# Kernel tuning notes

Measured on AMD Instinct MI355X. Metric: run time of the kernel, lower is better.

The kernel has to match this reference:

```python
import jax, jax.numpy as jnp
import numpy as np

B, S, W, D, H = 2, 2048, 32, 1024, 16

def setup_inputs() -> dict:
    key = jax.random.key(0)
    ks = jax.random.split(key, 8)
    scale = 0.02
    return {
        'q': jax.random.normal(ks[0], (B, S, D), jnp.float32),
        'k': jax.random.normal(ks[1], (B, S, W, D), jnp.float32),
        'v': jax.random.normal(ks[2], (B, S, W, D), jnp.float32),
        'Wq': jax.random.normal(ks[3], (D, D), jnp.float32) * scale,
        'bq': jnp.zeros((D,), jnp.float32),
        'Wk': jax.random.normal(ks[4], (D, D), jnp.float32) * scale,
        'bk': jnp.zeros((D,), jnp.float32),
        'Wv': jax.random.normal(ks[5], (D, D), jnp.float32) * scale,
        'bv': jnp.zeros((D,), jnp.float32),
        'Wo': jax.random.normal(ks[6], (D, D), jnp.float32) * scale,
        'bo': jnp.zeros((D,), jnp.float32),
        'num_heads': H,
    }

def reference(q, k, v, Wq, bq, Wk, bk, Wv, bv, Wo, bo, num_heads):
    b, s, d = q.shape
    w = k.shape[2]
    hd = d // num_heads
    # query: Linear -> view(B,S,H,1,hd) -> transpose(1,2) => (B,H,S,1,hd)
    qh = (q @ Wq.T + bq).reshape(b, s, num_heads, 1, hd).transpose(0, 2, 1, 3, 4)
    # key/value: Linear then RAW view (B,H,S,W,hd) -- faithful to torch .view (no head transpose)
    kh = (k @ Wk.T + bk).reshape(b, num_heads, s, w, hd)
    vh = (v @ Wv.T + bv).reshape(b, num_heads, s, w, hd)
    # scores: (B,H,S,1,W), scaled by sqrt(head_dim) (query.shape[-1] inside attention)
    scores = jnp.einsum('bhsid,bhswd->bhsiw', qh, kh) / jnp.sqrt(jnp.float32(hd))
    # Softmax(dim=1) normalizes over the HEAD axis -- faithful to the original
    attn = jax.nn.softmax(scores, axis=1)
    A = jnp.einsum('bhsiw,bhswd->bhsid', attn, vh)[:, :, :, 0, :]  # (B,H,S,hd)
    out = A.reshape(b, s, d)  # raw view, matches torch .view(B,S,D)
    return out @ Wo.T + bo
```

## Files before the change

kernel.cpp:

```cpp
#include <hip/hip_runtime.h>
#include <hip/hip_bf16.h>


#define DEVI __device__ __forceinline__

typedef __attribute__((ext_vector_type(8))) short bf16x8;
typedef __attribute__((ext_vector_type(4))) float f32x4;
typedef const __attribute__((address_space(1))) void* gvp;
typedef __attribute__((address_space(3))) void* lvp;

DEVI ushort f2bf(float f) {
  uint u = __float_as_uint(f);
  u = u + 0x7fffu + ((u >> 16) & 1u);
  return (ushort)(u >> 16);
}
DEVI float bf2f(ushort u) { return __uint_as_float(((uint)u) << 16); }

__global__ __launch_bounds__(256) void cast_kernel(const float* __restrict__ in,
                                                   ushort* __restrict__ out,
                                                   long n) {
  long i = ((long)blockIdx.x * 256 + threadIdx.x) * 8;
  const long stride = (long)gridDim.x * 256 * 8;
  for (; i < n; i += stride) {
    float4 a = *reinterpret_cast<const float4*>(in + i);
    float4 b = *reinterpret_cast<const float4*>(in + i + 4);
    ushort o[8];
    o[0] = f2bf(a.x); o[1] = f2bf(a.y); o[2] = f2bf(a.z); o[3] = f2bf(a.w);
    o[4] = f2bf(b.x); o[5] = f2bf(b.y); o[6] = f2bf(b.z); o[7] = f2bf(b.w);
    *reinterpret_cast<int4*>(out + i) = *reinterpret_cast<const int4*>(o);
  }
}

__global__ __launch_bounds__(512)
__attribute__((amdgpu_waves_per_eu(2, 2)))
void gemm_big(const float* __restrict__ Ag, const ushort* __restrict__ Wg,
              const float* __restrict__ bias, ushort* __restrict__ Cg) {
  constexpr int K = 1024;
  constexpr int NT = 32;
  constexpr int SLOT = 32768;
  __shared__ char lds[4 * SLOT];
  const int tid = threadIdx.x;
  const int lane = tid & 63;
  const int wave = tid >> 6;
  const int wm = wave >> 2;
  const int wn = wave & 3;
  const int d = blockIdx.x;
  const int bn = (d >> 3) & 3;
  const size_t bm = (size_t)(d & 7) * (gridDim.x >> 5) + (d >> 5);

  const ushort* bB = Wg + (size_t)bn * 256 * K;

  const int ar0 = tid >> 2;
  const int ac0 = (tid & 3) ^ ((ar0 >> 1) & 3);
  const float* pA0 = Ag + bm * 256 * K + (size_t)ar0 * K + ac0 * 8;
  const float* pA1 = pA0 + (size_t)128 * K;
  const ushort* bS0 = bB + (size_t)ar0 * K + ac0 * 8;
  const ushort* bS1 = bB + (size_t)(ar0 + 128) * K + ac0 * 8;
  const int adst0 = tid * 16;
  const int adst1 = tid * 16 + 8192;
  const int bdst0 = 16384 + tid * 16;
  const int bdst1 = 24576 + tid * 16;

  const int lm = lane & 15;
  const int cs = (lm >> 1) & 3;
  const int cSwz = ((lane >> 4) ^ cs) * 16;
  const int offA = lm * 64 + cSwz + wm * 8192;
  const int offB = 16384 + lm * 64 + cSwz + wn * 4096;
  const char* ldsc = (const char*)lds;

  f32x4 acc[8][4] = {};
  float4 st[4];

#define SB0 __builtin_amdgcn_sched_barrier(0)
#define AISS4(ktE)                                               \
  {                                                              \
    st[0] = *reinterpret_cast<const float4*>(pA0 + (ktE));       \
    st[1] = *reinterpret_cast<const float4*>(pA0 + (ktE) + 4);   \
    st[2] = *reinterpret_cast<const float4*>(pA1 + (ktE));       \
    st[3] = *reinterpret_cast<const float4*>(pA1 + (ktE) + 4);   \
  }
#define CVT4(base)                                                           \
  {                                                                          \
    uint w0, w1, w2, w3;                                                     \
    asm("v_cvt_pk_bf16_f32 %0,%1,%2" : "=v"(w0) : "v"(st[0].x), "v"(st[0].y)); \
    asm("v_cvt_pk_bf16_f32 %0,%1,%2" : "=v"(w1) : "v"(st[0].z), "v"(st[0].w)); \
    asm("v_cvt_pk_bf16_f32 %0,%1,%2" : "=v"(w2) : "v"(st[1].x), "v"(st[1].y)); \
    asm("v_cvt_pk_bf16_f32 %0,%1,%2" : "=v"(w3) : "v"(st[1].z), "v"(st[1].w)); \
    *reinterpret_cast<uint4*>(lds + (base) + adst0) = make_uint4(w0, w1, w2, w3); \
    asm("v_cvt_pk_bf16_f32 %0,%1,%2" : "=v"(w0) : "v"(st[2].x), "v"(st[2].y)); \
    asm("v_cvt_pk_bf16_f32 %0,%1,%2" : "=v"(w1) : "v"(st[2].z), "v"(st[2].w)); \
    asm("v_cvt_pk_bf16_f32 %0,%1,%2" : "=v"(w2) : "v"(st[3].x), "v"(st[3].y)); \
    asm("v_cvt_pk_bf16_f32 %0,%1,%2" : "=v"(w3) : "v"(st[3].z), "v"(st[3].w)); \
    *reinterpret_cast<uint4*>(lds + (base) + adst1) = make_uint4(w0, w1, w2, w3); \
  }
#define STGB(ktE, base)                                                        \
  {                                                                            \
    __builtin_amdgcn_global_load_lds((gvp)(bS0 + (ktE)),                       \
                                     (lvp)(lds + (base) + bdst0), 16, 0, 0);   \
    __builtin_amdgcn_global_load_lds((gvp)(bS1 + (ktE)),                       \
                                     (lvp)(lds + (base) + bdst1), 16, 0, 0);   \
  }

  AISS4(0);  SB0; CVT4(0 * SLOT); SB0;
  AISS4(32); SB0; CVT4(1 * SLOT); SB0;
  AISS4(64); SB0; CVT4(2 * SLOT); SB0;
  STGB(0, 0 * SLOT);
  STGB(32, 1 * SLOT);
  STGB(64, 2 * SLOT);
  AISS4(96); SB0;
  asm volatile("s_waitcnt vmcnt(0)" ::: "memory");
  asm volatile("s_waitcnt lgkmcnt(0)" ::: "memory");
  __builtin_amdgcn_s_barrier();
  SB0;

  int rdOff = 0, stOff = 3 * SLOT;
  for (int t = 0; t < NT; ++t) {
    if (t + 3 < NT) CVT4(stOff);
    if (t + 4 < NT) AISS4((t + 4) * 32);
    if (t + 3 < NT) STGB((t + 3) * 32, stOff);
    const char* pA = ldsc + rdOff + offA;
    const char* pB = ldsc + rdOff + offB;
    bf16x8 a[8], b[4];
#pragma unroll
    for (int fi = 0; fi < 8; ++fi)
      a[fi] = *reinterpret_cast<const bf16x8*>(pA + fi * 1024);
#pragma unroll
    for (int fj = 0; fj < 4; ++fj)
      b[fj] = *reinterpret_cast<const bf16x8*>(pB + fj * 1024);
    __builtin_amdgcn_s_setprio(1);
#pragma unroll
    for (int fi = 0; fi < 8; ++fi)
#pragma unroll
      for (int fj = 0; fj < 4; ++fj)
        acc[fi][fj] = __builtin_amdgcn_mfma_f32_16x16x32_bf16(a[fi], b[fj],
                                                              acc[fi][fj], 0, 0, 0);
    __builtin_amdgcn_s_setprio(0);
    if (t >= NT - 3 && t < NT - 1) {
      SB0;
      asm volatile("s_waitcnt vmcnt(0)" ::: "memory");
    }
    __builtin_amdgcn_s_barrier();
    rdOff = (rdOff == 3 * SLOT) ? 0 : rdOff + SLOT;
    stOff = (stOff == 3 * SLOT) ? 0 : stOff + SLOT;
  }
#undef AISS4
#undef CVT4
#undef STGB
#undef SB0

#pragma unroll
  for (int fi = 0; fi < 8; ++fi) {
#pragma unroll
    for (int fj = 0; fj < 4; ++fj) {
      int n = bn * 256 + wn * 64 + fj * 16 + lm;
      float bv = bias[n];
#pragma unroll
      for (int r = 0; r < 4; ++r) {
        size_t m = bm * 256 + wm * 128 + fi * 16 + ((lane >> 4) * 4) + r;
        Cg[m * 1024 + n] = f2bf(acc[fi][fj][r] + bv);
      }
    }
  }
}

template <typename TOUT>
__global__ __launch_bounds__(256) void gemm_lds(const ushort* __restrict__ Ag,
                                                const ushort* __restrict__ Wg,
                                                const float* __restrict__ bias,
                                                TOUT* __restrict__ Cg) {
  constexpr int K = 1024;
  __shared__ ushort lA[128 * 64];
  __shared__ ushort lB[128 * 64];
  const int tid = threadIdx.x;
  const int lane = tid & 63;
  const int wave = tid >> 6;
  const int wr = (wave >> 1) * 64;
  const int wc = (wave & 1) * 64;
  const int d = blockIdx.x;
  const int bn = (d >> 3) & 7;
  const size_t bm = (size_t)(d & 7) * (gridDim.x >> 6) + (d >> 6);

  const ushort* aB = Ag + bm * 128 * K;
  const ushort* bB = Wg + (size_t)bn * 128 * K;
  const int srow = wave * 32 + (lane >> 3);
  const int scol = ((lane & 7) ^ (lane >> 3)) * 8;
  char* lAc = (char*)lA;
  char* lBc = (char*)lB;

  f32x4 acc[4][4] = {};

  for (int kt = 0; kt < K; kt += 64) {
    __syncthreads();
#pragma unroll
    for (int c = 0; c < 4; ++c) {
      __builtin_amdgcn_global_load_lds(
          (gvp)(aB + (size_t)(srow + c * 8) * K + kt + scol),
          (lvp)(lAc + wave * 4096 + c * 1024), 16, 0, 0);
      __builtin_amdgcn_global_load_lds(
          (gvp)(bB + (size_t)(srow + c * 8) * K + kt + scol),
          (lvp)(lBc + wave * 4096 + c * 1024), 16, 0, 0);
    }
    __syncthreads();
#pragma unroll
    for (int kk = 0; kk < 2; ++kk) {
      bf16x8 af[4], bg[4];
#pragma unroll
      for (int fi = 0; fi < 4; ++fi) {
        int r = wr + fi * 16 + (lane & 15);
        int byte = (r * 128 + kk * 64 + ((lane >> 4) * 16)) ^ ((r & 7) << 4);
        af[fi] = *reinterpret_cast<const bf16x8*>(lAc + byte);
      }
#pragma unroll
      for (int fj = 0; fj < 4; ++fj) {
        int r = wc + fj * 16 + (lane & 15);
        int byte = (r * 128 + kk * 64 + ((lane >> 4) * 16)) ^ ((r & 7) << 4);
        bg[fj] = *reinterpret_cast<const bf16x8*>(lBc + byte);
      }
#pragma unroll
      for (int fi = 0; fi < 4; ++fi)
#pragma unroll
        for (int fj = 0; fj < 4; ++fj)
          acc[fi][fj] = __builtin_amdgcn_mfma_f32_16x16x32_bf16(af[fi], bg[fj],
                                                                acc[fi][fj], 0, 0, 0);
    }
  }
#pragma unroll
  for (int fi = 0; fi < 4; ++fi) {
#pragma unroll
    for (int fj = 0; fj < 4; ++fj) {
      int n = bn * 128 + wc + fj * 16 + (lane & 15);
      float bv = bias[n];
#pragma unroll
      for (int r = 0; r < 4; ++r) {
        size_t m = bm * 128 + wr + fi * 16 + ((lane >> 4) * 4) + r;
        float val = acc[fi][fj][r] + bv;
        if constexpr (sizeof(TOUT) == 2)
          reinterpret_cast<ushort*>(Cg)[m * 1024 + n] = f2bf(val);
        else
          reinterpret_cast<float*>(Cg)[m * 1024 + n] = val;
      }
    }
  }
}

template <typename TIN, typename TOUT>
__global__ __launch_bounds__(256) void gemm_bias(const TIN* __restrict__ Ag,
                                                 const float* __restrict__ Wg,
                                                 const float* __restrict__ bias,
                                                 TOUT* __restrict__ Cg) {
  constexpr int K = 1024;
  __shared__ char lA[128 * 64 * 2];
  __shared__ char lB[128 * 64 * 2];
  const int tid = threadIdx.x;
  const int lane = tid & 63;
  const int wave = tid >> 6;
  const int wr = (wave >> 1) * 64;
  const int wc = (wave & 1) * 64;
  const int bn = blockIdx.x;
  const size_t bm = blockIdx.y;

  const TIN* aBase = Ag + bm * 128 * K;
  const float* bBase = Wg + (size_t)bn * 128 * K;

  f32x4 acc[4][4] = {};

  for (int kt = 0; kt < K; kt += 64) {
    __syncthreads();
    if constexpr (sizeof(TIN) == 4) {
#pragma unroll
      for (int i = 0; i < 8; ++i) {
        int f = tid + i * 256;
        int row = f >> 4, c4 = f & 15;
        const float4 v = *reinterpret_cast<const float4*>(
            reinterpret_cast<const float*>(aBase) + (size_t)row * K + kt + c4 * 4);
        ushort4 pk;
        pk.x = f2bf(v.x); pk.y = f2bf(v.y); pk.z = f2bf(v.z); pk.w = f2bf(v.w);
        int byte = (row * 128 + c4 * 8) ^ ((row & 7) << 4);
        *reinterpret_cast<ushort4*>(lA + byte) = pk;
      }
    } else {
#pragma unroll
      for (int i = 0; i < 4; ++i) {
        int f = tid + i * 256;
        int row = f >> 3, c8 = f & 7;
        int4 v = *reinterpret_cast<const int4*>(
            reinterpret_cast<const ushort*>(aBase) + (size_t)row * K + kt + c8 * 8);
        int byte = (row * 128 + c8 * 16) ^ ((row & 7) << 4);
        *reinterpret_cast<int4*>(lA + byte) = v;
      }
    }
#pragma unroll
    for (int i = 0; i < 8; ++i) {
      int f = tid + i * 256;
      int row = f >> 4, c4 = f & 15;
      const float4 v =
          *reinterpret_cast<const float4*>(bBase + (size_t)row * K + kt + c4 * 4);
      ushort4 pk;
      pk.x = f2bf(v.x); pk.y = f2bf(v.y); pk.z = f2bf(v.z); pk.w = f2bf(v.w);
      int byte = (row * 128 + c4 * 8) ^ ((row & 7) << 4);
      *reinterpret_cast<ushort4*>(lB + byte) = pk;
    }
    __syncthreads();
#pragma unroll
    for (int kk = 0; kk < 2; ++kk) {
      bf16x8 af[4], bg[4];
#pragma unroll
      for (int fi = 0; fi < 4; ++fi) {
        int r = wr + fi * 16 + (lane & 15);
        int byte = (r * 128 + kk * 64 + ((lane >> 4) * 16)) ^ ((r & 7) << 4);
        af[fi] = *reinterpret_cast<const bf16x8*>(lA + byte);
      }
#pragma unroll
      for (int fj = 0; fj < 4; ++fj) {
        int r = wc + fj * 16 + (lane & 15);
        int byte = (r * 128 + kk * 64 + ((lane >> 4) * 16)) ^ ((r & 7) << 4);
        bg[fj] = *reinterpret_cast<const bf16x8*>(lB + byte);
      }
#pragma unroll
      for (int fi = 0; fi < 4; ++fi)
#pragma unroll
        for (int fj = 0; fj < 4; ++fj)
          acc[fi][fj] =
              __builtin_amdgcn_mfma_f32_16x16x32_bf16(af[fi], bg[fj], acc[fi][fj], 0, 0, 0);
    }
  }
#pragma unroll
  for (int fi = 0; fi < 4; ++fi) {
#pragma unroll
    for (int fj = 0; fj < 4; ++fj) {
      int n = bn * 128 + wc + fj * 16 + (lane & 15);
      float bv = bias[n];
#pragma unroll
      for (int r = 0; r < 4; ++r) {
        size_t m = bm * 128 + wr + fi * 16 + ((lane >> 4) * 4) + r;
        float val = acc[fi][fj][r] + bv;
        if constexpr (sizeof(TOUT) == 2)
          reinterpret_cast<ushort*>(Cg)[m * 1024 + n] = f2bf(val);
        else
          reinterpret_cast<float*>(Cg)[m * 1024 + n] = val;
      }
    }
  }
}

__global__ __launch_bounds__(512) void attn_kernel(const ushort* __restrict__ Q,
                                                   const ushort* __restrict__ Kl,
                                                   const ushort* __restrict__ Vl,
                                                   ushort* __restrict__ Aout) {
  const int bs = blockIdx.x;
  const int b = bs >> 11, sp = bs & 2047;
  const int tid = threadIdx.x;
  const int wave = tid >> 6, lane = tid & 63;

  __shared__ ushort qrow[1024];
  __shared__ float sc[16][32];
  __shared__ float attnw[16][32];
  __shared__ float mx[32], rinv[32];

  reinterpret_cast<uint*>(qrow)[tid] =
      reinterpret_cast<const uint*>(Q + (size_t)bs * 1024)[tid];
  __syncthreads();

  const int wp = lane & 31, half = lane >> 5;
#pragma unroll
  for (int hh = 0; hh < 2; ++hh) {
    const int h = wave * 2 + hh;
    const int s_k = h * 128 + (sp >> 4);
    const int w_k = (sp & 15) * 2 + (wp >> 4);
    const ushort* kp =
        Kl + (((size_t)(b * 2048 + s_k) * 32) + w_k) * 1024 + (wp & 15) * 64 + half * 32;
    const ushort* qp = qrow + h * 64 + half * 32;
    float dot = 0.f;
#pragma unroll
    for (int j = 0; j < 32; j += 8) {
      int4 kv = *reinterpret_cast<const int4*>(kp + j);
      int4 qv = *reinterpret_cast<const int4*>(qp + j);
      const ushort* ka = reinterpret_cast<const ushort*>(&kv);
      const ushort* qa = reinterpret_cast<const ushort*>(&qv);
#pragma unroll
      for (int t = 0; t < 8; ++t) dot += bf2f(ka[t]) * bf2f(qa[t]);
    }
    dot += __shfl_xor(dot, 32);
    if (half == 0) sc[h][wp] = dot * 0.125f;
  }
  __syncthreads();
  if (tid < 32) {
    float m = sc[0][tid];
#pragma unroll
    for (int h = 1; h < 16; ++h) m = fmaxf(m, sc[h][tid]);
    float s = 0.f;
#pragma unroll
    for (int h = 0; h < 16; ++h) s += __expf(sc[h][tid] - m);
    mx[tid] = m;
    rinv[tid] = 1.f / s;
  }
  __syncthreads();
  if (lane < 32) {
#pragma unroll
    for (int hh = 0; hh < 2; ++hh) {
      const int h = wave * 2 + hh;
      attnw[h][lane] = __expf(sc[h][lane] - mx[lane]) * rinv[lane];
    }
  }
  __syncthreads();
#pragma unroll
  for (int hh = 0; hh < 2; ++hh) {
    const int h = wave * 2 + hh;
    const int s_k = h * 128 + (sp >> 4);
    const size_t vb = (((size_t)(b * 2048 + s_k) * 32) + (sp & 15) * 2) * 1024;
    float a = 0.f;
#pragma unroll
    for (int w2 = 0; w2 < 32; ++w2) {
      float wgt = attnw[h][w2];
      a += wgt * bf2f(Vl[vb + (size_t)(w2 >> 4) * 1024 + (w2 & 15) * 64 + lane]);
    }
    Aout[(((size_t)(b * 16 + h)) * 2048 + sp) * 64 + lane] = f2bf(a);
  }
}

extern "C" void kernel_launch(void* const* d_in, const int* in_sizes, int n_in,
                              void* d_out, int out_size, void* d_ws, size_t ws_size,
                              hipStream_t stream) {
  const float* q = (const float*)d_in[0];
  const float* k = (const float*)d_in[1];
  const float* v = (const float*)d_in[2];
  const float* Wq = (const float*)d_in[3];
  const float* bq = (const float*)d_in[4];
  const float* Wk = (const float*)d_in[5];
  const float* bk = (const float*)d_in[6];
  const float* Wv = (const float*)d_in[7];
  const float* bv = (const float*)d_in[8];
  const float* Wo = (const float*)d_in[9];
  const float* bo = (const float*)d_in[10];
  float* out = (float*)d_out;

  char* ws = (char*)d_ws;
  const size_t MB = 1u << 20;
  ushort* Qlin = (ushort*)ws;
  ushort* Aws  = (ushort*)(ws + 8 * MB);
  ushort* wkbf = (ushort*)(ws + 16 * MB);
  ushort* wvbf = (ushort*)(ws + 18 * MB);
  ushort* wqbf = (ushort*)(ws + 20 * MB);
  ushort* wobf = (ushort*)(ws + 22 * MB);
  ushort* qbf  = (ushort*)(ws + 24 * MB);
  ushort* Klin = (ushort*)(ws + 32 * MB);
  ushort* Vlin = (ushort*)(ws + 288 * MB);
  const bool full = ws_size >= 800 * MB;

  if (full) {
    cast_kernel<<<dim3(512), 256, 0, stream>>>(Wq, wqbf, 1048576L);
    cast_kernel<<<dim3(512), 256, 0, stream>>>(Wk, wkbf, 1048576L);
    cast_kernel<<<dim3(512), 256, 0, stream>>>(Wv, wvbf, 1048576L);
    cast_kernel<<<dim3(512), 256, 0, stream>>>(Wo, wobf, 1048576L);
    cast_kernel<<<dim3(2048), 256, 0, stream>>>(q, qbf, 4194304L);
    gemm_lds<ushort><<<dim3(256), 256, 0, stream>>>(qbf, wqbf, bq, Qlin);
    gemm_big<<<dim3(2048), 512, 0, stream>>>(k, wkbf, bk, Klin);
    gemm_big<<<dim3(2048), 512, 0, stream>>>(v, wvbf, bv, Vlin);
    attn_kernel<<<dim3(4096), dim3(512), 0, stream>>>(Qlin, Klin, Vlin, Aws);
    gemm_lds<float><<<dim3(256), 256, 0, stream>>>(Aws, wobf, bo, out);
  } else {
    gemm_bias<float, ushort><<<dim3(8, 32), 256, 0, stream>>>(q, Wq, bq, Qlin);
    gemm_bias<float, ushort><<<dim3(8, 1024), 256, 0, stream>>>(k, Wk, bk, Klin);
    gemm_bias<float, ushort><<<dim3(8, 1024), 256, 0, stream>>>(v, Wv, bv, Vlin);
    attn_kernel<<<dim3(4096), dim3(512), 0, stream>>>(Qlin, Klin, Vlin, Aws);
    gemm_bias<ushort, float><<<dim3(8, 32), 256, 0, stream>>>(Aws, Wo, bo, out);
  }
}
```

Baseline: 928.2 us.

## Deepen A-operand register prefetch with rotating triple staging buffers in GEMM

Replaces the single fp32 staging register set for the A operand with three rotating sets (sa/sb/sc). Global loads for A are now issued five tiles ahead instead of four, and the bf16 conversion and LDS store run after the MFMA block rather than before it. The main loop is unrolled by three to rotate the sets, with the tile count hardcoded to 32, and the prologue waits only for part of the outstanding loads. The aim is to hide global load latency and the conversion work behind the matrix math, at the cost of more VGPRs and a fragile dependence on the tile count and vmcnt bookkeeping.

```diff
diff --git a/kernel.cpp b/kernel.cpp
--- a/kernel.cpp
+++ b/kernel.cpp
@@ -69,28 +69,28 @@
   const char* ldsc = (const char*)lds;
 
   f32x4 acc[8][4] = {};
-  float4 st[4];
+  float4 sa[4], sb[4], sc[4];
 
 #define SB0 __builtin_amdgcn_sched_barrier(0)
-#define AISS4(ktE)                                               \
-  {                                                              \
-    st[0] = *reinterpret_cast<const float4*>(pA0 + (ktE));       \
-    st[1] = *reinterpret_cast<const float4*>(pA0 + (ktE) + 4);   \
-    st[2] = *reinterpret_cast<const float4*>(pA1 + (ktE));       \
-    st[3] = *reinterpret_cast<const float4*>(pA1 + (ktE) + 4);   \
-  }
-#define CVT4(base)                                                           \
-  {                                                                          \
-    uint w0, w1, w2, w3;                                                     \
-    asm("v_cvt_pk_bf16_f32 %0,%1,%2" : "=v"(w0) : "v"(st[0].x), "v"(st[0].y)); \
-    asm("v_cvt_pk_bf16_f32 %0,%1,%2" : "=v"(w1) : "v"(st[0].z), "v"(st[0].w)); \
-    asm("v_cvt_pk_bf16_f32 %0,%1,%2" : "=v"(w2) : "v"(st[1].x), "v"(st[1].y)); \
-    asm("v_cvt_pk_bf16_f32 %0,%1,%2" : "=v"(w3) : "v"(st[1].z), "v"(st[1].w)); \
+#define AISS4(set, ktE)                                           \
+  {                                                               \
+    set[0] = *reinterpret_cast<const float4*>(pA0 + (ktE));       \
+    set[1] = *reinterpret_cast<const float4*>(pA0 + (ktE) + 4);   \
+    set[2] = *reinterpret_cast<const float4*>(pA1 + (ktE));       \
+    set[3] = *reinterpret_cast<const float4*>(pA1 + (ktE) + 4);   \
+  }
+#define CVT4(set, base)                                                          \
+  {                                                                              \
+    uint w0, w1, w2, w3;                                                         \
+    asm("v_cvt_pk_bf16_f32 %0,%1,%2" : "=v"(w0) : "v"(set[0].x), "v"(set[0].y)); \
+    asm("v_cvt_pk_bf16_f32 %0,%1,%2" : "=v"(w1) : "v"(set[0].z), "v"(set[0].w)); \
+    asm("v_cvt_pk_bf16_f32 %0,%1,%2" : "=v"(w2) : "v"(set[1].x), "v"(set[1].y)); \
+    asm("v_cvt_pk_bf16_f32 %0,%1,%2" : "=v"(w3) : "v"(set[1].z), "v"(set[1].w)); \
     *reinterpret_cast<uint4*>(lds + (base) + adst0) = make_uint4(w0, w1, w2, w3); \
-    asm("v_cvt_pk_bf16_f32 %0,%1,%2" : "=v"(w0) : "v"(st[2].x), "v"(st[2].y)); \
-    asm("v_cvt_pk_bf16_f32 %0,%1,%2" : "=v"(w1) : "v"(st[2].z), "v"(st[2].w)); \
-    asm("v_cvt_pk_bf16_f32 %0,%1,%2" : "=v"(w2) : "v"(st[3].x), "v"(st[3].y)); \
-    asm("v_cvt_pk_bf16_f32 %0,%1,%2" : "=v"(w3) : "v"(st[3].z), "v"(st[3].w)); \
+    asm("v_cvt_pk_bf16_f32 %0,%1,%2" : "=v"(w0) : "v"(set[2].x), "v"(set[2].y)); \
+    asm("v_cvt_pk_bf16_f32 %0,%1,%2" : "=v"(w1) : "v"(set[2].z), "v"(set[2].w)); \
+    asm("v_cvt_pk_bf16_f32 %0,%1,%2" : "=v"(w2) : "v"(set[3].x), "v"(set[3].y)); \
+    asm("v_cvt_pk_bf16_f32 %0,%1,%2" : "=v"(w3) : "v"(set[3].z), "v"(set[3].w)); \
     *reinterpret_cast<uint4*>(lds + (base) + adst1) = make_uint4(w0, w1, w2, w3); \
   }
 #define STGB(ktE, base)                                                        \
@@ -101,48 +101,60 @@
                                      (lvp)(lds + (base) + bdst1), 16, 0, 0);   \
   }
 
-  AISS4(0);  SB0; CVT4(0 * SLOT); SB0;
-  AISS4(32); SB0; CVT4(1 * SLOT); SB0;
-  AISS4(64); SB0; CVT4(2 * SLOT); SB0;
+  AISS4(sa, 0);  SB0; CVT4(sa, 0 * SLOT); SB0;
+  AISS4(sa, 32); SB0; CVT4(sa, 1 * SLOT); SB0;
+  AISS4(sa, 64); SB0; CVT4(sa, 2 * SLOT); SB0;
   STGB(0, 0 * SLOT);
   STGB(32, 1 * SLOT);
   STGB(64, 2 * SLOT);
-  AISS4(96); SB0;
-  asm volatile("s_waitcnt vmcnt(0)" ::: "memory");
+  AISS4(sa, 96);
+  AISS4(sb, 128);
+  SB0;
+  asm volatile("s_waitcnt vmcnt(12)" ::: "memory");
   asm volatile("s_waitcnt lgkmcnt(0)" ::: "memory");
   __builtin_amdgcn_s_barrier();
   SB0;
 
   int rdOff = 0, stOff = 3 * SLOT;
-  for (int t = 0; t < NT; ++t) {
-    if (t + 3 < NT) CVT4(stOff);
-    if (t + 4 < NT) AISS4((t + 4) * 32);
-    if (t + 3 < NT) STGB((t + 3) * 32, stOff);
-    const char* pA = ldsc + rdOff + offA;
-    const char* pB = ldsc + rdOff + offB;
-    bf16x8 a[8], b[4];
-#pragma unroll
-    for (int fi = 0; fi < 8; ++fi)
-      a[fi] = *reinterpret_cast<const bf16x8*>(pA + fi * 1024);
-#pragma unroll
-    for (int fj = 0; fj < 4; ++fj)
-      b[fj] = *reinterpret_cast<const bf16x8*>(pB + fj * 1024);
-    __builtin_amdgcn_s_setprio(1);
-#pragma unroll
-    for (int fi = 0; fi < 8; ++fi)
-#pragma unroll
-      for (int fj = 0; fj < 4; ++fj)
-        acc[fi][fj] = __builtin_amdgcn_mfma_f32_16x16x32_bf16(a[fi], b[fj],
-                                                              acc[fi][fj], 0, 0, 0);
-    __builtin_amdgcn_s_setprio(0);
-    if (t >= NT - 3 && t < NT - 1) {
-      SB0;
-      asm volatile("s_waitcnt vmcnt(0)" ::: "memory");
-    }
-    __builtin_amdgcn_s_barrier();
-    rdOff = (rdOff == 3 * SLOT) ? 0 : rdOff + SLOT;
-    stOff = (stOff == 3 * SLOT) ? 0 : stOff + SLOT;
-  }
+
+#define TILE(tt, CS, IS)                                                     \
+  {                                                                          \
+    const char* pA = ldsc + rdOff + offA;                                    \
+    const char* pB = ldsc + rdOff + offB;                                    \
+    bf16x8 a[8], b[4];                                                       \
+    _Pragma("unroll") for (int fi = 0; fi < 8; ++fi)                         \
+        a[fi] = *reinterpret_cast<const bf16x8*>(pA + fi * 1024);            \
+    _Pragma("unroll") for (int fj = 0; fj < 4; ++fj)                         \
+        b[fj] = *reinterpret_cast<const bf16x8*>(pB + fj * 1024);            \
+    if ((tt) + 3 < NT) STGB(((tt) + 3) * 32, stOff);                         \
+    if ((tt) + 5 < NT) AISS4(IS, ((tt) + 5) * 32);                           \
+    SB0;                                                                     \
+    __builtin_amdgcn_s_setprio(1);                                           \
+    _Pragma("unroll") for (int fi = 0; fi < 8; ++fi)                         \
+        _Pragma("unroll") for (int fj = 0; fj < 4; ++fj)                     \
+            acc[fi][fj] = __builtin_amdgcn_mfma_f32_16x16x32_bf16(           \
+                a[fi], b[fj], acc[fi][fj], 0, 0, 0);                         \
+    __builtin_amdgcn_s_setprio(0);                                           \
+    SB0;                                                                     \
+    if ((tt) + 3 < NT) CVT4(CS, stOff);                                      \
+    if ((tt) >= NT - 3 && (tt) < NT - 1) {                                   \
+      SB0;                                                                   \
+      asm volatile("s_waitcnt vmcnt(0)" ::: "memory");                       \
+    }                                                                        \
+    __builtin_amdgcn_s_barrier();                                            \
+    rdOff = (rdOff == 3 * SLOT) ? 0 : rdOff + SLOT;                          \
+    stOff = (stOff == 3 * SLOT) ? 0 : stOff + SLOT;                          \
+  }
+
+#pragma unroll 1
+  for (int tb = 0; tb < 30; tb += 3) {
+    TILE(tb, sa, sc);
+    TILE(tb + 1, sb, sa);
+    TILE(tb + 2, sc, sb);
+  }
+  TILE(30, sa, sc);
+  TILE(31, sb, sa);
+#undef TILE
 #undef AISS4
 #undef CVT4
 #undef STGB
```

Result: slower. 1.052 ms (+13.3%).
